# Kernel tuning notes

Hardware: AMD Instinct MI355X
Metric: run time of the kernel (lower is better)

Reference implementation:

```python
import jax, jax.numpy as jnp
import numpy as np

B, S, HID = 1, 4096, 2048
H, KV, D = 16, 8, 128
N_REP = H // KV
SCALING = float(128 ** -0.5)   # query_pre_attn_scalar ** -0.5
SOFTCAP = 50.0
WINDOW = 1024
NEG = -1e9


def setup_inputs() -> dict:
    key = jax.random.key(0)
    ks = jax.random.split(key, 6)
    hidden_states = jax.random.normal(ks[0], (B, S, HID), dtype=jnp.float32)
    Wq = jax.random.normal(ks[1], (HID, H * D), dtype=jnp.float32) * 0.02
    Wk = jax.random.normal(ks[2], (HID, KV * D), dtype=jnp.float32) * 0.02
    Wv = jax.random.normal(ks[3], (HID, KV * D), dtype=jnp.float32) * 0.02
    Wo = jax.random.normal(ks[4], (H * D, HID), dtype=jnp.float32) * 0.02
    # RoPE tables [1, S, D]
    inv_freq = 1.0 / (10000.0 ** (jnp.arange(0, D, 2, dtype=jnp.float32) / D))
    freqs = jnp.outer(jnp.arange(S, dtype=jnp.float32), inv_freq)   # [S, D/2]
    emb = jnp.concatenate([freqs, freqs], axis=-1)                  # [S, D]
    cos = jnp.cos(emb)[None]
    sin = jnp.sin(emb)[None]
    # causal + sliding-window additive mask [1, 1, S, S]
    i = jnp.arange(S)[:, None]
    j = jnp.arange(S)[None, :]
    allowed = (j <= i) & ((i - j) < WINDOW)
    attention_mask = jnp.where(allowed, 0.0, NEG).astype(jnp.float32)[None, None]
    return {"hidden_states": hidden_states, "cos": cos, "sin": sin,
            "attention_mask": attention_mask, "Wq": Wq, "Wk": Wk, "Wv": Wv, "Wo": Wo}


def _rotate_half(x):
    x1, x2 = jnp.split(x, 2, axis=-1)
    return jnp.concatenate([-x2, x1], axis=-1)


def reference(hidden_states, cos, sin, attention_mask, Wq, Wk, Wv, Wo):
    b, s, _ = hidden_states.shape
    # projections -> [B, heads, S, D]
    q = (hidden_states @ Wq).reshape(b, s, H, D).transpose(0, 2, 1, 3)
    k = (hidden_states @ Wk).reshape(b, s, KV, D).transpose(0, 2, 1, 3)
    v = (hidden_states @ Wv).reshape(b, s, KV, D).transpose(0, 2, 1, 3)
    # RoPE (unsqueeze_dim=1)
    c = cos[:, None]  # [B, 1, S, D]
    sn = sin[:, None]
    q = q * c + _rotate_half(q) * sn
    k = k * c + _rotate_half(k) * sn
    # repeat_kv (GQA)
    k = jnp.repeat(k, N_REP, axis=1)
    v = jnp.repeat(v, N_REP, axis=1)
    # scores with softcap + mask
    scores = jnp.einsum('bhqd,bhkd->bhqk', q, k) * SCALING
    scores = jnp.tanh(scores / SOFTCAP) * SOFTCAP
    scores = scores + attention_mask
    attn = jax.nn.softmax(scores.astype(jnp.float32), axis=-1).astype(q.dtype)
    out = jnp.einsum('bhqk,bhkd->bhqd', attn, v)
    out = out.transpose(0, 2, 1, 3).reshape(b, s, H * D)
    return out @ Wo
```

## Files before the change

kernel.cpp:

```cpp
#include <hip/hip_runtime.h>

#define S 4096
#define HID 2048
#define NH 16
#define NKV 8
#define HD 128
#define WINDOW 1024
#define SCALING 0.08838834764831845f
#define SOFTCAP 50.0f

typedef __bf16 bf16x8 __attribute__((ext_vector_type(8)));
typedef __bf16 bf16x4 __attribute__((ext_vector_type(4)));
typedef float f32x4 __attribute__((ext_vector_type(4)));

__device__ inline void gll16(const void* g, void* l) {
  __builtin_amdgcn_global_load_lds((const __attribute__((address_space(1))) void*)g,
                                   (__attribute__((address_space(3))) void*)l, 16, 0, 0);
}

__global__ void prep_all(const float* __restrict__ hs, __bf16* __restrict__ hsb,
                         const float* __restrict__ Wq, const float* __restrict__ Wk,
                         const float* __restrict__ Wv, const float* __restrict__ Wo,
                         __bf16* __restrict__ wqkvT, __bf16* __restrict__ woT) {
  int b = blockIdx.x;
  int t = threadIdx.x;
  if (b < 8192) {
    int i = b * 256 + t;
    float4 v = ((const float4*)hs)[i];
    bf16x4 o;
    o[0] = (__bf16)v.x; o[1] = (__bf16)v.y; o[2] = (__bf16)v.z; o[3] = (__bf16)v.w;
    ((bf16x4*)hsb)[i] = o;
    return;
  }
  __shared__ float tile[64][65];
  int y = b - 8192;
  int k0 = (y & 31) * 64;
  int wy = y >> 5;
  const float* src; __bf16* dst; int Nsrc, c0, perm, n0;
  if (wy < 32)      { src = Wq; dst = wqkvT; Nsrc = 2048; c0 = wy * 64;        perm = 1; n0 = wy * 64; }
  else if (wy < 48) { src = Wk; dst = wqkvT; Nsrc = 1024; c0 = (wy - 32) * 64; perm = 1; n0 = 2048 + (wy - 32) * 64; }
  else if (wy < 64) { src = Wv; dst = wqkvT; Nsrc = 1024; c0 = (wy - 48) * 64; perm = 0; n0 = 3072 + (wy - 48) * 64; }
  else              { src = Wo; dst = woT;   Nsrc = 2048; c0 = (wy - 64) * 64; perm = 0; n0 = (wy - 64) * 64; }
#pragma unroll
  for (int e = 0; e < 16; ++e) {
    int f = e * 256 + t; int r = f >> 6, c = f & 63;
    tile[r][c] = src[(size_t)(k0 + r) * Nsrc + c0 + c];
  }
  __syncthreads();
#pragma unroll
  for (int e = 0; e < 16; ++e) {
    int f = e * 256 + t; int r = f >> 6, c = f & 63;
    int n = n0 + r;
    if (perm) {
      int d = n & 127, o = d >> 4;
      int g = (o < 4) ? (o * 2) : ((o - 4) * 2 + 1);
      n = (n & ~127) | (g << 4) | (d & 15);
    }
    dst[(size_t)n * 2048 + k0 + c] = (__bf16)tile[c][r];
  }
}

__global__ __launch_bounds__(256) void gemm_qkv(const __bf16* __restrict__ A,
                                                const __bf16* __restrict__ B,
                                                __bf16* __restrict__ qr,
                                                __bf16* __restrict__ kr,
                                                __bf16* __restrict__ vt,
                                                const float* __restrict__ cosp,
                                                const float* __restrict__ sinp) {
  __shared__ __align__(16) __bf16 As[128 * 64];
  __shared__ __align__(16) __bf16 Bs[128 * 64];
  const int K = 2048;
  int m0 = blockIdx.x * 128, n0 = blockIdx.y * 128;
  int t = threadIdx.x;
  int lane = t & 63, wave = t >> 6;
  int wm = wave & 1, wn = wave >> 1;
  int quad = lane >> 4, l16 = lane & 15;

  f32x4 acc[4][4] = {};

  const __bf16* Abase = A + (size_t)m0 * K;
  const __bf16* Bbase = B + (size_t)n0 * K;

  for (int kk = 0; kk < K; kk += 64) {
    __syncthreads();
#pragma unroll
    for (int i = 0; i < 4; ++i) {
      int idx = i * 256 + t;
      int row = idx >> 3, c = idx & 7;
      int g = (c ^ (row & 7)) * 8;
      gll16(Abase + (size_t)row * K + kk + g, &As[idx * 8]);
      gll16(Bbase + (size_t)row * K + kk + g, &Bs[idx * 8]);
    }
    __syncthreads();
#pragma unroll
    for (int ks = 0; ks < 64; ks += 32) {
      bf16x8 af[4], bfr[4];
#pragma unroll
      for (int i = 0; i < 4; ++i) {
        int row = wm * 64 + i * 16 + l16;
        af[i] = *(const bf16x8*)&As[row * 64 + (((quad + (ks >> 3)) ^ (row & 7)) * 8)];
      }
#pragma unroll
      for (int j = 0; j < 4; ++j) {
        int row = wn * 64 + j * 16 + l16;
        bfr[j] = *(const bf16x8*)&Bs[row * 64 + (((quad + (ks >> 3)) ^ (row & 7)) * 8)];
      }
#pragma unroll
      for (int i = 0; i < 4; ++i)
#pragma unroll
        for (int j = 0; j < 4; ++j)
          acc[i][j] = __builtin_amdgcn_mfma_f32_16x16x32_bf16(af[i], bfr[j], acc[i][j], 0, 0, 0);
    }
  }

  if (n0 < 3072) {
    __bf16* dst = (n0 < 2048) ? (qr + (size_t)(n0 >> 7) * S * 128)
                              : (kr + (size_t)((n0 - 2048) >> 7) * S * 128);
#pragma unroll
    for (int i = 0; i < 4; ++i)
#pragma unroll
      for (int r = 0; r < 4; ++r) {
        int row = m0 + wm * 64 + i * 16 + quad * 4 + r;
#pragma unroll
        for (int jp = 0; jp < 2; ++jp) {
          int ifr = (wn * 2 + jp) * 16 + l16;
          float c = cosp[(size_t)row * 128 + ifr];
          float sn = sinp[(size_t)row * 128 + ifr];
          float lo = acc[i][2 * jp][r], hi = acc[i][2 * jp + 1][r];
          dst[(size_t)row * 128 + wn * 64 + jp * 32 + l16]      = (__bf16)(lo * c - hi * sn);
          dst[(size_t)row * 128 + wn * 64 + jp * 32 + 16 + l16] = (__bf16)(hi * c + lo * sn);
        }
      }
  } else {
    int vc0 = n0 - 3072;
#pragma unroll
    for (int i = 0; i < 4; ++i)
#pragma unroll
      for (int j = 0; j < 4; ++j) {
        int row_base = m0 + wm * 64 + i * 16 + quad * 4;
        int col = vc0 + wn * 64 + j * 16 + l16;
        bf16x4 ov;
#pragma unroll
        for (int r = 0; r < 4; ++r) ov[r] = (__bf16)acc[i][j][r];
        *(bf16x4*)&vt[(size_t)col * S + row_base] = ov;
      }
  }
}

template <typename OutT>
__global__ __launch_bounds__(256) void gemm_bt(const __bf16* __restrict__ A,
                                               const __bf16* __restrict__ B,
                                               OutT* __restrict__ C, int N, int K) {
  __shared__ __align__(16) __bf16 As[128 * 64];
  __shared__ __align__(16) __bf16 Bs[128 * 64];
  int m0 = blockIdx.x * 128, n0 = blockIdx.y * 128;
  int t = threadIdx.x;
  int lane = t & 63, wave = t >> 6;
  int wm = wave & 1, wn = wave >> 1;
  int quad = lane >> 4, l16 = lane & 15;

  f32x4 acc[4][4] = {};

  const __bf16* Abase = A + (size_t)m0 * K;
  const __bf16* Bbase = B + (size_t)n0 * K;

  for (int kk = 0; kk < K; kk += 64) {
    __syncthreads();
#pragma unroll
    for (int i = 0; i < 4; ++i) {
      int idx = i * 256 + t;
      int row = idx >> 3, c = idx & 7;
      int g = (c ^ (row & 7)) * 8;
      gll16(Abase + (size_t)row * K + kk + g, &As[idx * 8]);
      gll16(Bbase + (size_t)row * K + kk + g, &Bs[idx * 8]);
    }
    __syncthreads();
#pragma unroll
    for (int ks = 0; ks < 64; ks += 32) {
      bf16x8 af[4], bfr[4];
#pragma unroll
      for (int i = 0; i < 4; ++i) {
        int row = wm * 64 + i * 16 + l16;
        af[i] = *(const bf16x8*)&As[row * 64 + (((quad + (ks >> 3)) ^ (row & 7)) * 8)];
      }
#pragma unroll
      for (int j = 0; j < 4; ++j) {
        int row = wn * 64 + j * 16 + l16;
        bfr[j] = *(const bf16x8*)&Bs[row * 64 + (((quad + (ks >> 3)) ^ (row & 7)) * 8)];
      }
#pragma unroll
      for (int i = 0; i < 4; ++i)
#pragma unroll
        for (int j = 0; j < 4; ++j)
          acc[i][j] = __builtin_amdgcn_mfma_f32_16x16x32_bf16(af[i], bfr[j], acc[i][j], 0, 0, 0);
    }
  }
#pragma unroll
  for (int i = 0; i < 4; ++i)
#pragma unroll
    for (int j = 0; j < 4; ++j)
#pragma unroll
      for (int r = 0; r < 4; ++r) {
        int row = m0 + wm * 64 + i * 16 + quad * 4 + r;
        int col = n0 + wn * 64 + j * 16 + l16;
        C[(size_t)row * N + col] = (OutT)acc[i][j][r];
      }
}

__global__ __launch_bounds__(512) void attn(const __bf16* __restrict__ qr,
                                            const __bf16* __restrict__ kr,
                                            const __bf16* __restrict__ vt,
                                            __bf16* __restrict__ ao) {
  __shared__ __align__(16) __bf16 Ks[2][64 * 128];
  __shared__ __align__(16) __bf16 Vs[3][128 * 64];

  int kvh = blockIdx.x;
  int q0 = blockIdx.y * 128;
  int t = threadIdx.x, lane = t & 63, wave = t >> 6;
  int quad = lane >> 4, l16 = lane & 15;
  int h = kvh * 2 + (wave & 1);
  int qbase = q0 + (wave >> 1) * 32;

  bf16x8 qf[2][4];
#pragma unroll
  for (int mi = 0; mi < 2; ++mi) {
    const __bf16* qptr = qr + ((size_t)h * S + qbase + mi * 16 + l16) * 128;
#pragma unroll
    for (int ks = 0; ks < 4; ++ks)
      qf[mi][ks] = *(const bf16x8*)&qptr[ks * 32 + quad * 8];
  }

  f32x4 o[2][8] = {};
  float lpart[2] = {0.f, 0.f};

  int lo = q0 - (WINDOW - 1); if (lo < 0) lo = 0;
  int kt_begin = (lo / 64) * 64;
  int kt_end = q0 + 128;
  int NT = (kt_end - kt_begin) >> 6;

  const __bf16* kbase0 = kr + (size_t)kvh * S * 128;
  const __bf16* vbase0 = vt + (size_t)kvh * 128 * S;

  float4 kreg[2];
  float2 vregA[2], vregB[2];

  auto load_regs = [&](int kt) {
    const __bf16* kb = kbase0 + (size_t)kt * 128;
    const __bf16* vb = vbase0 + kt;
#pragma unroll
    for (int i = 0; i < 2; ++i) {
      int off = i * 512 + t;
      kreg[i] = *(const float4*)(kb + (size_t)off * 8);
      int r = off >> 3, c = off & 7;
      int base0 = 32 * (c >> 2) + 4 * (c & 3);
      vregA[i] = *(const float2*)(vb + (size_t)r * S + base0);
      vregB[i] = *(const float2*)(vb + (size_t)r * S + base0 + 16);
    }
  };
  auto write_lds = [&](int kslot, int vslot) {
#pragma unroll
    for (int i = 0; i < 2; ++i) {
      int off = i * 512 + t;
      { int r = off >> 4, c = off & 15;
        *(float4*)&Ks[kslot][r * 128 + ((c ^ (r & 15)) * 8)] = kreg[i]; }
      { int r = off >> 3, c = off & 7;
        float4 v = {vregA[i].x, vregA[i].y, vregB[i].x, vregB[i].y};
        *(float4*)&Vs[vslot][r * 64 + ((c ^ (r & 7)) * 8)] = v; }
    }
  };

  const float XS = SCALING / SOFTCAP;
  f32x4 sA[2][4], sB[2][4];

  auto activ = [&](int kt0) {
    return !(kt0 > qbase + 31 || kt0 + 63 < qbase - (WINDOW - 1));
  };

  auto step = [&](int tt, f32x4 (&SC)[2][4], f32x4 (&SP)[2][4], int vr, int vw) {
    if (tt < NT) {
      int kt0 = kt_begin + tt * 64;
      if (activ(kt0)) {
        int kslot = tt & 1;
#pragma unroll
        for (int mi = 0; mi < 2; ++mi)
#pragma unroll
          for (int nt = 0; nt < 4; ++nt) SC[mi][nt] = {};
#pragma unroll
        for (int nt = 0; nt < 4; ++nt) {
#pragma unroll
          for (int ks = 0; ks < 4; ++ks) {
            bf16x8 kf = *(const bf16x8*)&Ks[kslot][(nt * 16 + l16) * 128 + (((ks * 4 + quad) ^ l16) * 8)];
            SC[0][nt] = __builtin_amdgcn_mfma_f32_16x16x32_bf16(kf, qf[0][ks], SC[0][nt], 0, 0, 0);
            SC[1][nt] = __builtin_amdgcn_mfma_f32_16x16x32_bf16(kf, qf[1][ks], SC[1][nt], 0, 0, 0);
          }
        }
      }
    }

    if (tt > 0) {
      int kt0c = kt_begin + (tt - 1) * 64;
      if (activ(kt0c)) {
        bf16x4 pk[2][4];
        bool interior = (kt0c + 63 <= qbase) && (kt0c >= qbase + 31 - (WINDOW - 1));
#pragma unroll
        for (int mi = 0; mi < 2; ++mi) {
          int irow = qbase + mi * 16 + l16;
#pragma unroll
          for (int nt = 0; nt < 4; ++nt)
#pragma unroll
            for (int r = 0; r < 4; ++r) {
              float x = SP[mi][nt][r] * XS;
              x = fminf(fmaxf(x, -0.25f), 0.25f);
              float x2 = x * x;
              float th = x * fmaf(x2, fmaf(x2, 0.13333333f, -0.33333333f), 1.0f);
              float pp = __builtin_amdgcn_exp2f(fmaf(th, 72.134752f, -72.134752f));
              if (!interior) {
                int j = kt0c + nt * 16 + quad * 4 + r;
                bool ok = (j <= irow) && (irow - j < WINDOW);
                pp = ok ? pp : 0.0f;
              }
              lpart[mi] += pp;
              pk[mi][nt][r] = (__bf16)pp;
            }
        }

        bf16x8 pB[2][2];
#pragma unroll
        for (int mi = 0; mi < 2; ++mi)
#pragma unroll
          for (int ks = 0; ks < 2; ++ks)
#pragma unroll
            for (int e = 0; e < 4; ++e) {
              pB[mi][ks][e]     = pk[mi][2 * ks][e];
              pB[mi][ks][4 + e] = pk[mi][2 * ks + 1][e];
            }

#pragma unroll
        for (int dt = 0; dt < 8; ++dt) {
          int row = dt * 16 + l16;
#pragma unroll
          for (int ks = 0; ks < 2; ++ks) {
            bf16x8 vf = *(const bf16x8*)&Vs[vr][row * 64 + (((ks * 4 + quad) ^ (l16 & 7)) * 8)];
#pragma unroll
            for (int mi = 0; mi < 2; ++mi)
              o[mi][dt] = __builtin_amdgcn_mfma_f32_16x16x32_bf16(vf, pB[mi][ks], o[mi][dt], 0, 0, 0);
          }
        }
      }
    }

    if (tt + 1 < NT) write_lds((tt + 1) & 1, vw);
    if (tt + 2 < NT) load_regs(kt_begin + (tt + 2) * 64);
    __syncthreads();
  };

  load_regs(kt_begin);
  write_lds(0, 0);
  if (NT > 1) load_regs(kt_begin + 64);
  __syncthreads();

  int vw = 1, vr = 2;
  for (int tt = 0; tt < NT; tt += 2) {
    step(tt, sA, sB, vr, vw);
    if (++vw == 3) vw = 0; if (++vr == 3) vr = 0;
    step(tt + 1, sB, sA, vr, vw);
    if (++vw == 3) vw = 0; if (++vr == 3) vr = 0;
  }
  step(NT, sA, sB, vr, vw);

#pragma unroll
  for (int mi = 0; mi < 2; ++mi) {
    float ls = lpart[mi];
    ls += __shfl_xor(ls, 16);
    ls += __shfl_xor(ls, 32);
    float inv = 1.f / ls;
    int row = qbase + mi * 16 + l16;
    __bf16* dst = ao + (size_t)row * (NH * HD) + h * HD + quad * 4;
#pragma unroll
    for (int dt = 0; dt < 8; ++dt) {
      bf16x4 ov;
#pragma unroll
      for (int r = 0; r < 4; ++r) ov[r] = (__bf16)(o[mi][dt][r] * inv);
      *(bf16x4*)(dst + dt * 16) = ov;
    }
  }
}

extern "C" void kernel_launch(void* const* d_in, const int* in_sizes, int n_in,
                              void* d_out, int out_size, void* d_ws, size_t ws_size,
                              hipStream_t stream) {
  const float* hs   = (const float*)d_in[0];
  const float* cosp = (const float*)d_in[1];
  const float* sinp = (const float*)d_in[2];
  const float* Wq = (const float*)d_in[4];
  const float* Wk = (const float*)d_in[5];
  const float* Wv = (const float*)d_in[6];
  const float* Wo = (const float*)d_in[7];
  float* out = (float*)d_out;

  char* w = (char*)d_ws;
  __bf16* hsb   = (__bf16*)w; w += (size_t)S * HID * 2;
  __bf16* wqkvT = (__bf16*)w; w += (size_t)4096 * 2048 * 2;
  __bf16* woT   = (__bf16*)w; w += (size_t)2048 * 2048 * 2;
  __bf16* qr    = (__bf16*)w; w += (size_t)NH * S * HD * 2;
  __bf16* kr    = (__bf16*)w; w += (size_t)NKV * S * HD * 2;
  __bf16* vtb   = (__bf16*)w; w += (size_t)NKV * HD * S * 2;
  __bf16* ao    = (__bf16*)w; w += (size_t)S * 2048 * 2;

  prep_all<<<8192 + 3072, 256, 0, stream>>>(hs, hsb, Wq, Wk, Wv, Wo, wqkvT, woT);

  gemm_qkv<<<dim3(32, 32), 256, 0, stream>>>(hsb, wqkvT, qr, kr, vtb, cosp, sinp);

  attn<<<dim3(NKV, 32), 512, 0, stream>>>(qr, kr, vtb, ao);

  gemm_bt<float><<<dim3(32, 16), 256, 0, stream>>>(ao, woT, out, 2048, 2048);
}
```

Before: 360.9 us.

## Rework QKV GEMM into 256x256 tiles with 4-stage async LDS pipeline

The QKV projection GEMM moves from 128x128 tiles with 256 threads and a two-barrier synchronous loop to 256x256 tiles with 512 threads (8 waves). It uses a 4-buffer LDS ring with a prefetch distance of two, vmcnt-based waits, a single barrier per k-step and raised wave priority around the MFMA block. The goal is to hide global-load latency and raise data reuse per tile. In exchange the grid shrinks to 256 blocks, which leaves some CUs idle on MI355X. Register and LDS pressure also grow, with 128 accumulator floats per lane and 128 KB of LDS, which may limit occupancy.

```diff
diff --git a/kernel.cpp b/kernel.cpp
--- a/kernel.cpp
+++ b/kernel.cpp
@@ -60,88 +60,104 @@
   }
 }
 
-__global__ __launch_bounds__(256) void gemm_qkv(const __bf16* __restrict__ A,
-                                                const __bf16* __restrict__ B,
-                                                __bf16* __restrict__ qr,
-                                                __bf16* __restrict__ kr,
-                                                __bf16* __restrict__ vt,
-                                                const float* __restrict__ cosp,
-                                                const float* __restrict__ sinp) {
-  __shared__ __align__(16) __bf16 As[128 * 64];
-  __shared__ __align__(16) __bf16 Bs[128 * 64];
+__global__ __launch_bounds__(512, 2) void gemm_qkv(const __bf16* __restrict__ A,
+                                                   const __bf16* __restrict__ B,
+                                                   __bf16* __restrict__ qr,
+                                                   __bf16* __restrict__ kr,
+                                                   __bf16* __restrict__ vt,
+                                                   const float* __restrict__ cosp,
+                                                   const float* __restrict__ sinp) {
+  __shared__ __align__(16) __bf16 As[4][256 * 32];
+  __shared__ __align__(16) __bf16 Bs[4][256 * 32];
   const int K = 2048;
-  int m0 = blockIdx.x * 128, n0 = blockIdx.y * 128;
+  const int NT = K / 32;
+  int m0 = blockIdx.x * 256, n0 = blockIdx.y * 256;
   int t = threadIdx.x;
   int lane = t & 63, wave = t >> 6;
   int wm = wave & 1, wn = wave >> 1;
   int quad = lane >> 4, l16 = lane & 15;
 
-  f32x4 acc[4][4] = {};
+  f32x4 acc[8][4] = {};
 
   const __bf16* Abase = A + (size_t)m0 * K;
   const __bf16* Bbase = B + (size_t)n0 * K;
 
-  for (int kk = 0; kk < K; kk += 64) {
-    __syncthreads();
-#pragma unroll
-    for (int i = 0; i < 4; ++i) {
-      int idx = i * 256 + t;
-      int row = idx >> 3, c = idx & 7;
-      int g = (c ^ (row & 7)) * 8;
-      gll16(Abase + (size_t)row * K + kk + g, &As[idx * 8]);
-      gll16(Bbase + (size_t)row * K + kk + g, &Bs[idx * 8]);
-    }
-    __syncthreads();
-#pragma unroll
-    for (int ks = 0; ks < 64; ks += 32) {
-      bf16x8 af[4], bfr[4];
-#pragma unroll
-      for (int i = 0; i < 4; ++i) {
-        int row = wm * 64 + i * 16 + l16;
-        af[i] = *(const bf16x8*)&As[row * 64 + (((quad + (ks >> 3)) ^ (row & 7)) * 8)];
-      }
-#pragma unroll
-      for (int j = 0; j < 4; ++j) {
-        int row = wn * 64 + j * 16 + l16;
-        bfr[j] = *(const bf16x8*)&Bs[row * 64 + (((quad + (ks >> 3)) ^ (row & 7)) * 8)];
-      }
-#pragma unroll
-      for (int i = 0; i < 4; ++i)
-#pragma unroll
-        for (int j = 0; j < 4; ++j)
-          acc[i][j] = __builtin_amdgcn_mfma_f32_16x16x32_bf16(af[i], bfr[j], acc[i][j], 0, 0, 0);
-    }
+  auto stage = [&](int tt) {
+    int buf = tt & 3;
+    int kk = tt * 32;
+#pragma unroll
+    for (int j = 0; j < 2; ++j) {
+      int L = j * 512 + t;
+      int r = L >> 2, cp = L & 3;
+      int c = cp ^ (r & 3);
+      gll16(Abase + (size_t)r * K + kk + c * 8, &As[buf][L * 8]);
+      gll16(Bbase + (size_t)r * K + kk + c * 8, &Bs[buf][L * 8]);
+    }
+  };
+
+  stage(0);
+  stage(1);
+  asm volatile("s_waitcnt vmcnt(4)" ::: "memory");
+  __builtin_amdgcn_s_barrier();
+
+  int cst = (quad ^ (l16 & 3)) * 8;
+
+  for (int tt = 0; tt < NT; ++tt) {
+    if (tt + 2 < NT) stage(tt + 2);
+
+    int buf = tt & 3;
+    bf16x8 af[8], bf[4];
+#pragma unroll
+    for (int mi = 0; mi < 8; ++mi)
+      af[mi] = *(const bf16x8*)&As[buf][(wm * 128 + mi * 16 + l16) * 32 + cst];
+#pragma unroll
+    for (int ni = 0; ni < 4; ++ni)
+      bf[ni] = *(const bf16x8*)&Bs[buf][(wn * 64 + ni * 16 + l16) * 32 + cst];
+
+    __builtin_amdgcn_s_setprio(1);
+#pragma unroll
+    for (int mi = 0; mi < 8; ++mi)
+#pragma unroll
+      for (int ni = 0; ni < 4; ++ni)
+        acc[mi][ni] = __builtin_amdgcn_mfma_f32_16x16x32_bf16(af[mi], bf[ni], acc[mi][ni], 0, 0, 0);
+    __builtin_amdgcn_s_setprio(0);
+
+    if (tt + 2 < NT) { asm volatile("s_waitcnt vmcnt(4)" ::: "memory"); }
+    else             { asm volatile("s_waitcnt vmcnt(0)" ::: "memory"); }
+    __builtin_amdgcn_s_barrier();
   }
 
   if (n0 < 3072) {
-    __bf16* dst = (n0 < 2048) ? (qr + (size_t)(n0 >> 7) * S * 128)
-                              : (kr + (size_t)((n0 - 2048) >> 7) * S * 128);
-#pragma unroll
-    for (int i = 0; i < 4; ++i)
+    int nf = n0 + wn * 64;
+    __bf16* dst = (n0 < 2048) ? (qr + (size_t)(nf >> 7) * S * 128)
+                              : (kr + (size_t)((nf - 2048) >> 7) * S * 128);
+    int colb = nf & 64;
+#pragma unroll
+    for (int mi = 0; mi < 8; ++mi)
 #pragma unroll
       for (int r = 0; r < 4; ++r) {
-        int row = m0 + wm * 64 + i * 16 + quad * 4 + r;
+        int row = m0 + wm * 128 + mi * 16 + quad * 4 + r;
 #pragma unroll
         for (int jp = 0; jp < 2; ++jp) {
-          int ifr = (wn * 2 + jp) * 16 + l16;
+          int ifr = ((2 * (wn & 1) + jp) & 3) * 16 + l16;
           float c = cosp[(size_t)row * 128 + ifr];
           float sn = sinp[(size_t)row * 128 + ifr];
-          float lo = acc[i][2 * jp][r], hi = acc[i][2 * jp + 1][r];
-          dst[(size_t)row * 128 + wn * 64 + jp * 32 + l16]      = (__bf16)(lo * c - hi * sn);
-          dst[(size_t)row * 128 + wn * 64 + jp * 32 + 16 + l16] = (__bf16)(hi * c + lo * sn);
+          float lo = acc[mi][2 * jp][r], hi = acc[mi][2 * jp + 1][r];
+          dst[(size_t)row * 128 + colb + jp * 32 + l16]      = (__bf16)(lo * c - hi * sn);
+          dst[(size_t)row * 128 + colb + jp * 32 + 16 + l16] = (__bf16)(hi * c + lo * sn);
         }
       }
   } else {
     int vc0 = n0 - 3072;
 #pragma unroll
-    for (int i = 0; i < 4; ++i)
-#pragma unroll
-      for (int j = 0; j < 4; ++j) {
-        int row_base = m0 + wm * 64 + i * 16 + quad * 4;
-        int col = vc0 + wn * 64 + j * 16 + l16;
+    for (int mi = 0; mi < 8; ++mi)
+#pragma unroll
+      for (int ni = 0; ni < 4; ++ni) {
+        int row_base = m0 + wm * 128 + mi * 16 + quad * 4;
+        int col = vc0 + wn * 64 + ni * 16 + l16;
         bf16x4 ov;
 #pragma unroll
-        for (int r = 0; r < 4; ++r) ov[r] = (__bf16)acc[i][j][r];
+        for (int r = 0; r < 4; ++r) ov[r] = (__bf16)acc[mi][ni][r];
         *(bf16x4*)&vt[(size_t)col * S + row_base] = ov;
       }
   }
@@ -409,7 +425,7 @@
 
   prep_all<<<8192 + 3072, 256, 0, stream>>>(hs, hsb, Wq, Wk, Wv, Wo, wqkvT, woT);
 
-  gemm_qkv<<<dim3(32, 32), 256, 0, stream>>>(hsb, wqkvT, qr, kr, vtb, cosp, sinp);
+  gemm_qkv<<<dim3(16, 16), 512, 0, stream>>>(hsb, wqkvT, qr, kr, vtb, cosp, sinp);
 
   attn<<<dim3(NKV, 32), 512, 0, stream>>>(qr, kr, vtb, ao);
 
```

Measured after the change: 375.7 us. 4.1% more time.
